# Performance work log

Measured on AMD Instinct MI355X. Metric: run time of the kernel, lower is better.

The kernel has to match this reference:

```python
import jax, jax.numpy as jnp
import numpy as np

N_NODES = 100000


def setup_inputs() -> dict:
    key = jax.random.key(0)
    k1, k2, k3, k4 = jax.random.split(key, 4)
    E = 1600000
    D_IN, D_OUT = 256, 256
    feat = jax.random.normal(k1, (N_NODES, D_IN), dtype=jnp.float32)
    src = jax.random.randint(k2, (E,), 0, N_NODES, dtype=jnp.int32)
    dst = jax.random.randint(k3, (E,), 0, N_NODES, dtype=jnp.int32)
    # xavier_uniform-like init for weight
    limit = np.sqrt(6.0 / (D_IN + D_OUT)).astype(np.float32)
    weight = jax.random.uniform(k4, (D_IN, D_OUT), dtype=jnp.float32,
                                minval=-limit, maxval=limit)
    bias = jnp.zeros((D_OUT,), dtype=jnp.float32)
    return {"feat": feat, "src": src, "dst": dst, "weight": weight, "bias": bias}


def reference(feat, src, dst, weight, bias):
    ones = jnp.ones(src.shape[0], dtype=feat.dtype)
    # out_degrees: number of outgoing edges per node (src counts)
    out_deg = jax.ops.segment_sum(ones, src, num_segments=N_NODES)
    # in_degrees: number of incoming edges per node (dst counts)
    in_deg = jax.ops.segment_sum(ones, dst, num_segments=N_NODES)
    # norm == 'both': pre-scale by out_deg^-0.5
    pre = jnp.power(jnp.clip(out_deg, 1.0), -0.5)[:, None]  # [N,1]
    h = feat * pre
    # message passing: copy_src + sum over incoming edges (SpMM)
    agg = jax.ops.segment_sum(h[src], dst, num_segments=N_NODES)  # [N, D_in]
    # dense projection
    rst = agg @ weight  # [N, D_out]
    # post-scale by in_deg^-0.5
    post = jnp.power(jnp.clip(in_deg, 1.0), -0.5)[:, None]
    rst = rst * post + bias
    return rst
```

## Files before the change

kernel.cpp:

```cpp
#include <hip/hip_runtime.h>
#include <hip/hip_bf16.h>
#include <stdint.h>


using short8  = __attribute__((ext_vector_type(8))) short;
using floatx4 = __attribute__((ext_vector_type(4))) float;
using ushort8 = __attribute__((ext_vector_type(8))) unsigned short;

static __device__ __forceinline__ unsigned short f32_to_bf16(float f) {
    unsigned int u = __float_as_uint(f);
    u += 0x7FFFu + ((u >> 16) & 1u);
    return (unsigned short)(u >> 16);
}
static __device__ __forceinline__ float bf2f(unsigned short u) {
    return __uint_as_float((unsigned int)u << 16);
}

__global__ void k_deg(const int* __restrict__ src, const int* __restrict__ dst,
                      int E, int* __restrict__ outc, int* __restrict__ inc) {
    int i = blockIdx.x * blockDim.x + threadIdx.x;
    if (i < E) {
        atomicAdd(&outc[src[i]], 1);
        atomicAdd(&inc[dst[i]], 1);
    }
}

__global__ void k_off(const int* __restrict__ inc, int N, int* __restrict__ total,
                      int* __restrict__ cursor) {
    __shared__ int ss[256];
    __shared__ int sbase;
    int t = threadIdx.x;
    int i = blockIdx.x * 256 + t;
    int d = (i < N) ? inc[i] : 0;
    int v = d;
    ss[t] = v;
    __syncthreads();
    for (int off = 1; off < 256; off <<= 1) {
        int u = (t >= off) ? ss[t - off] : 0;
        __syncthreads();
        v += u;
        ss[t] = v;
        __syncthreads();
    }
    if (t == 255) sbase = atomicAdd(total, v);
    __syncthreads();
    if (i < N) cursor[i] = sbase + (v - d);
}

__global__ void k_fill(const int* __restrict__ src, const int* __restrict__ dst,
                       int E, int* __restrict__ cursor, int* __restrict__ eidx) {
    int i = blockIdx.x * blockDim.x + threadIdx.x;
    if (i < E) {
        int p = atomicAdd(&cursor[dst[i]], 1);
        eidx[p] = src[i];
    }
}

__global__ void k_wt(const float* __restrict__ W, unsigned short* __restrict__ WT) {
    int i = blockIdx.x * blockDim.x + threadIdx.x;
    int n = i >> 8, k = i & 255;
    WT[n * 256 + k] = f32_to_bf16(W[(size_t)k * 256 + n]);
}

__global__ void __launch_bounds__(512, 4)
k_gemm(const float* __restrict__ feat, const int* __restrict__ outc,
       const unsigned short* __restrict__ WT, int N,
       unsigned short* __restrict__ z) {
    __shared__ unsigned short ldsB[256 * 128];

    int tid  = threadIdx.x;
    int wave = tid >> 6;
    int lane = tid & 63;
    int rl   = lane & 15;
    int g    = lane >> 4;
    int wm0  = blockIdx.x * 128 + wave * 16;
    int rowc = min(wm0 + rl, N - 1);
    float p  = rsqrtf((float)max(outc[rowc], 1));
    const float4* arow = (const float4*)(feat + (size_t)rowc * 256);
    int smask = (rl & 7) << 4;

    floatx4 acc[16];
#pragma unroll
    for (int n = 0; n < 16; ++n) acc[n] = (floatx4){0.f, 0.f, 0.f, 0.f};

#pragma unroll
    for (int h = 0; h < 2; ++h) {
        if (h) __syncthreads();
#pragma unroll
        for (int i = 0; i < 8; ++i) {
            int c    = i * 512 + tid;
            int r2   = c >> 4;
            int colb = (c & 15) << 4;
            ushort8 v = *(const ushort8*)(WT + r2 * 256 + h * 128 + (colb >> 1));
            int dst = r2 * 128 + ((colb ^ ((r2 & 7) << 4)) >> 1);
            *(ushort8*)(&ldsB[dst]) = v;
        }
        __syncthreads();

#pragma unroll
        for (int k2 = 0; k2 < 4; ++k2) {
            float4 v0 = arow[h * 32 + k2 * 8 + g * 2];
            float4 v1 = arow[h * 32 + k2 * 8 + g * 2 + 1];
            short8 a;
            a[0] = (short)f32_to_bf16(v0.x * p);
            a[1] = (short)f32_to_bf16(v0.y * p);
            a[2] = (short)f32_to_bf16(v0.z * p);
            a[3] = (short)f32_to_bf16(v0.w * p);
            a[4] = (short)f32_to_bf16(v1.x * p);
            a[5] = (short)f32_to_bf16(v1.y * p);
            a[6] = (short)f32_to_bf16(v1.z * p);
            a[7] = (short)f32_to_bf16(v1.w * p);
            int cb = (k2 * 64 + g * 16) ^ smask;
#pragma unroll
            for (int n = 0; n < 16; ++n) {
                short8 b = *(const short8*)(&ldsB[(n * 16 + rl) * 128 + (cb >> 1)]);
                acc[n] = __builtin_amdgcn_mfma_f32_16x16x32_bf16(a, b, acc[n], 0, 0, 0);
            }
        }
    }

#pragma unroll
    for (int i = 0; i < 4; ++i) {
        int rw = wm0 + g * 4 + i;
        if (rw < N) {
            ushort8 u0, u1;
#pragma unroll
            for (int j = 0; j < 8; ++j) {
                u0[j] = f32_to_bf16(acc[j][i]);
                u1[j] = f32_to_bf16(acc[8 + j][i]);
            }
            *(ushort8*)(z + (size_t)rw * 256 + rl * 16)     = u0;
            *(ushort8*)(z + (size_t)rw * 256 + rl * 16 + 8) = u1;
        }
    }
}

__global__ void k_agg(const unsigned short* __restrict__ z,
                      const int* __restrict__ cursor, const int* __restrict__ inc,
                      const int* __restrict__ eidx, const float* __restrict__ bias,
                      int N, float* __restrict__ out) {
    int node = blockIdx.x * 4 + (threadIdx.x >> 6);
    if (node >= N) return;
    int lane = threadIdx.x & 63;
    int half = lane >> 5;
    int l = lane & 31;
    int deg = inc[node];
    const int* ep = eidx + (cursor[node] - deg);

    float acc[8];
#pragma unroll
    for (int j = 0; j < 8; ++j) acc[j] = 0.f;

    int e = 0;
    for (; e + 1 < deg; e += 2) {
        int s = ep[e + half];
        ushort8 v = *(const ushort8*)(z + (size_t)s * 256 + l * 8);
#pragma unroll
        for (int j = 0; j < 8; ++j) acc[j] += bf2f(v[j]);
    }
    if (e < deg && half == 0) {
        int s = ep[e];
        ushort8 v = *(const ushort8*)(z + (size_t)s * 256 + l * 8);
#pragma unroll
        for (int j = 0; j < 8; ++j) acc[j] += bf2f(v[j]);
    }
#pragma unroll
    for (int j = 0; j < 8; ++j) acc[j] += __shfl_xor(acc[j], 32);

    float post = rsqrtf((float)max(deg, 1));
#pragma unroll
    for (int jj = 0; jj < 4; ++jj) {
        int pcol = l * 8 + half * 4 + jj;
        int c = ((pcol & 15) << 4) | (pcol >> 4);
        out[(size_t)node * 256 + c] = acc[half * 4 + jj] * post + bias[c];
    }
}

extern "C" void kernel_launch(void* const* d_in, const int* in_sizes, int n_in,
                              void* d_out, int out_size, void* d_ws, size_t ws_size,
                              hipStream_t stream) {
    const float* feat = (const float*)d_in[0];
    const int*   src  = (const int*)d_in[1];
    const int*   dst  = (const int*)d_in[2];
    const float* W    = (const float*)d_in[3];
    const float* bias = (const float*)d_in[4];
    float* out = (float*)d_out;

    const int D = 256;
    int N = in_sizes[0] / D;
    int E = in_sizes[1];

    char* ws = (char*)d_ws;
    size_t off = 0;
    auto alloc = [&](size_t bytes) -> void* {
        void* p = ws + off;
        off += (bytes + 255) & ~(size_t)255;
        return p;
    };
    int*            cnt    = (int*)alloc(((size_t)2 * N + 64) * sizeof(int));
    int*            outc   = cnt;
    int*            inc    = cnt + N;
    int*            total  = cnt + 2 * N;
    int*            cursor = (int*)alloc((size_t)N * sizeof(int));
    int*            eidx   = (int*)alloc((size_t)E * sizeof(int));
    unsigned short* z      = (unsigned short*)alloc((size_t)N * D * sizeof(unsigned short));
    unsigned short* WT     = (unsigned short*)alloc((size_t)D * D * sizeof(unsigned short));
    (void)ws_size;

    hipMemsetAsync(cnt, 0, ((size_t)2 * N + 64) * sizeof(int), stream);

    k_deg <<<(E + 255) / 256, 256, 0, stream>>>(src, dst, E, outc, inc);
    k_off <<<(N + 255) / 256, 256, 0, stream>>>(inc, N, total, cursor);
    k_fill<<<(E + 255) / 256, 256, 0, stream>>>(src, dst, E, cursor, eidx);
    k_wt  <<<(D * D) / 256, 256, 0, stream>>>(W, WT);
    k_gemm<<<(N + 127) / 128, 512, 0, stream>>>(feat, outc, WT, N, z);
    k_agg <<<(N + 3) / 4, 256, 0, stream>>>(z, cursor, inc, eidx, bias, N, out);
}
```

Before: 566.8 us.

## Vectorize edge kernels, split aggregation by column half, change z layout and nontemporal IO

```diff
diff --git a/kernel.cpp b/kernel.cpp
--- a/kernel.cpp
+++ b/kernel.cpp
@@ -5,6 +5,7 @@
 
 using short8  = __attribute__((ext_vector_type(8))) short;
 using floatx4 = __attribute__((ext_vector_type(4))) float;
+using floatx2 = __attribute__((ext_vector_type(2))) float;
 using ushort8 = __attribute__((ext_vector_type(8))) unsigned short;
 
 static __device__ __forceinline__ unsigned short f32_to_bf16(float f) {
@@ -19,9 +20,23 @@
 __global__ void k_deg(const int* __restrict__ src, const int* __restrict__ dst,
                       int E, int* __restrict__ outc, int* __restrict__ inc) {
     int i = blockIdx.x * blockDim.x + threadIdx.x;
-    if (i < E) {
-        atomicAdd(&outc[src[i]], 1);
-        atomicAdd(&inc[dst[i]], 1);
+    int b = i * 4;
+    if (b + 3 < E) {
+        int4 s = *(const int4*)(src + b);
+        int4 d = *(const int4*)(dst + b);
+        atomicAdd(&outc[s.x], 1);
+        atomicAdd(&outc[s.y], 1);
+        atomicAdd(&outc[s.z], 1);
+        atomicAdd(&outc[s.w], 1);
+        atomicAdd(&inc[d.x], 1);
+        atomicAdd(&inc[d.y], 1);
+        atomicAdd(&inc[d.z], 1);
+        atomicAdd(&inc[d.w], 1);
+    } else {
+        for (int j = b; j < E; ++j) {
+            atomicAdd(&outc[src[j]], 1);
+            atomicAdd(&inc[dst[j]], 1);
+        }
     }
 }
 
@@ -50,9 +65,23 @@
 __global__ void k_fill(const int* __restrict__ src, const int* __restrict__ dst,
                        int E, int* __restrict__ cursor, int* __restrict__ eidx) {
     int i = blockIdx.x * blockDim.x + threadIdx.x;
-    if (i < E) {
-        int p = atomicAdd(&cursor[dst[i]], 1);
-        eidx[p] = src[i];
+    int b = i * 4;
+    if (b + 3 < E) {
+        int4 s = *(const int4*)(src + b);
+        int4 d = *(const int4*)(dst + b);
+        int p0 = atomicAdd(&cursor[d.x], 1);
+        int p1 = atomicAdd(&cursor[d.y], 1);
+        int p2 = atomicAdd(&cursor[d.z], 1);
+        int p3 = atomicAdd(&cursor[d.w], 1);
+        eidx[p0] = s.x;
+        eidx[p1] = s.y;
+        eidx[p2] = s.z;
+        eidx[p3] = s.w;
+    } else {
+        for (int j = b; j < E; ++j) {
+            int p = atomicAdd(&cursor[dst[j]], 1);
+            eidx[p] = src[j];
+        }
     }
 }
 
@@ -76,7 +105,7 @@
     int wm0  = blockIdx.x * 128 + wave * 16;
     int rowc = min(wm0 + rl, N - 1);
     float p  = rsqrtf((float)max(outc[rowc], 1));
-    const float4* arow = (const float4*)(feat + (size_t)rowc * 256);
+    const floatx4* arow = (const floatx4*)(feat + (size_t)rowc * 256);
     int smask = (rl & 7) << 4;
 
     floatx4 acc[16];
@@ -99,17 +128,17 @@
 
 #pragma unroll
         for (int k2 = 0; k2 < 4; ++k2) {
-            float4 v0 = arow[h * 32 + k2 * 8 + g * 2];
-            float4 v1 = arow[h * 32 + k2 * 8 + g * 2 + 1];
+            floatx4 v0 = __builtin_nontemporal_load(arow + h * 32 + k2 * 8 + g * 2);
+            floatx4 v1 = __builtin_nontemporal_load(arow + h * 32 + k2 * 8 + g * 2 + 1);
             short8 a;
-            a[0] = (short)f32_to_bf16(v0.x * p);
-            a[1] = (short)f32_to_bf16(v0.y * p);
-            a[2] = (short)f32_to_bf16(v0.z * p);
-            a[3] = (short)f32_to_bf16(v0.w * p);
-            a[4] = (short)f32_to_bf16(v1.x * p);
-            a[5] = (short)f32_to_bf16(v1.y * p);
-            a[6] = (short)f32_to_bf16(v1.z * p);
-            a[7] = (short)f32_to_bf16(v1.w * p);
+            a[0] = (short)f32_to_bf16(v0[0] * p);
+            a[1] = (short)f32_to_bf16(v0[1] * p);
+            a[2] = (short)f32_to_bf16(v0[2] * p);
+            a[3] = (short)f32_to_bf16(v0[3] * p);
+            a[4] = (short)f32_to_bf16(v1[0] * p);
+            a[5] = (short)f32_to_bf16(v1[1] * p);
+            a[6] = (short)f32_to_bf16(v1[2] * p);
+            a[7] = (short)f32_to_bf16(v1[3] * p);
             int cb = (k2 * 64 + g * 16) ^ smask;
 #pragma unroll
             for (int n = 0; n < 16; ++n) {
@@ -120,17 +149,12 @@
     }
 
 #pragma unroll
-    for (int i = 0; i < 4; ++i) {
-        int rw = wm0 + g * 4 + i;
-        if (rw < N) {
-            ushort8 u0, u1;
-#pragma unroll
-            for (int j = 0; j < 8; ++j) {
-                u0[j] = f32_to_bf16(acc[j][i]);
-                u1[j] = f32_to_bf16(acc[8 + j][i]);
-            }
-            *(ushort8*)(z + (size_t)rw * 256 + rl * 16)     = u0;
-            *(ushort8*)(z + (size_t)rw * 256 + rl * 16 + 8) = u1;
+    for (int n = 0; n < 16; ++n) {
+        int c = n * 16 + rl;
+#pragma unroll
+        for (int i = 0; i < 4; ++i) {
+            int rw = wm0 + g * 4 + i;
+            if (rw < N) z[(size_t)rw * 256 + c] = f32_to_bf16(acc[n][i]);
         }
     }
 }
@@ -141,39 +165,51 @@
                       int N, float* __restrict__ out) {
     int node = blockIdx.x * 4 + (threadIdx.x >> 6);
     if (node >= N) return;
+    int h    = blockIdx.y;
     int lane = threadIdx.x & 63;
-    int half = lane >> 5;
-    int l = lane & 31;
-    int deg = inc[node];
+    int q    = lane >> 4;
+    int sl   = lane & 15;
+    int deg  = inc[node];
     const int* ep = eidx + (cursor[node] - deg);
-
-    float acc[8];
-#pragma unroll
-    for (int j = 0; j < 8; ++j) acc[j] = 0.f;
+    const unsigned short* zh = z + h * 128 + sl * 8;
+
+    float accA[8], accB[8];
+#pragma unroll
+    for (int j = 0; j < 8; ++j) { accA[j] = 0.f; accB[j] = 0.f; }
 
     int e = 0;
-    for (; e + 1 < deg; e += 2) {
-        int s = ep[e + half];
-        ushort8 v = *(const ushort8*)(z + (size_t)s * 256 + l * 8);
-#pragma unroll
-        for (int j = 0; j < 8; ++j) acc[j] += bf2f(v[j]);
-    }
-    if (e < deg && half == 0) {
-        int s = ep[e];
-        ushort8 v = *(const ushort8*)(z + (size_t)s * 256 + l * 8);
-#pragma unroll
-        for (int j = 0; j < 8; ++j) acc[j] += bf2f(v[j]);
-    }
-#pragma unroll
-    for (int j = 0; j < 8; ++j) acc[j] += __shfl_xor(acc[j], 32);
+    for (; e + 8 <= deg; e += 8) {
+        int s0 = ep[e + q];
+        int s1 = ep[e + 4 + q];
+        ushort8 v0 = *(const ushort8*)(zh + (size_t)s0 * 256);
+        ushort8 v1 = *(const ushort8*)(zh + (size_t)s1 * 256);
+#pragma unroll
+        for (int j = 0; j < 8; ++j) {
+            accA[j] += bf2f(v0[j]);
+            accB[j] += bf2f(v1[j]);
+        }
+    }
+    for (; e < deg; e += 4) {
+        if (e + q < deg) {
+            int s = ep[e + q];
+            ushort8 v = *(const ushort8*)(zh + (size_t)s * 256);
+#pragma unroll
+            for (int j = 0; j < 8; ++j) accA[j] += bf2f(v[j]);
+        }
+    }
+#pragma unroll
+    for (int j = 0; j < 8; ++j) accA[j] += accB[j];
+#pragma unroll
+    for (int j = 0; j < 8; ++j) accA[j] += __shfl_xor(accA[j], 16);
+#pragma unroll
+    for (int j = 0; j < 8; ++j) accA[j] += __shfl_xor(accA[j], 32);
 
     float post = rsqrtf((float)max(deg, 1));
-#pragma unroll
-    for (int jj = 0; jj < 4; ++jj) {
-        int pcol = l * 8 + half * 4 + jj;
-        int c = ((pcol & 15) << 4) | (pcol >> 4);
-        out[(size_t)node * 256 + c] = acc[half * 4 + jj] * post + bias[c];
-    }
+    int c = h * 128 + sl * 8 + q * 2;
+    floatx2 o;
+    o[0] = accA[q * 2 + 0] * post + bias[c];
+    o[1] = accA[q * 2 + 1] * post + bias[c + 1];
+    __builtin_nontemporal_store(o, (floatx2*)(out + (size_t)node * 256 + c));
 }
 
 extern "C" void kernel_launch(void* const* d_in, const int* in_sizes, int n_in,
@@ -209,10 +245,11 @@
 
     hipMemsetAsync(cnt, 0, ((size_t)2 * N + 64) * sizeof(int), stream);
 
-    k_deg <<<(E + 255) / 256, 256, 0, stream>>>(src, dst, E, outc, inc);
+    int tE4 = (E + 3) / 4;
+    k_deg <<<(tE4 + 255) / 256, 256, 0, stream>>>(src, dst, E, outc, inc);
     k_off <<<(N + 255) / 256, 256, 0, stream>>>(inc, N, total, cursor);
-    k_fill<<<(E + 255) / 256, 256, 0, stream>>>(src, dst, E, cursor, eidx);
+    k_fill<<<(tE4 + 255) / 256, 256, 0, stream>>>(src, dst, E, cursor, eidx);
     k_wt  <<<(D * D) / 256, 256, 0, stream>>>(W, WT);
     k_gemm<<<(N + 127) / 128, 512, 0, stream>>>(feat, outc, WT, N, z);
-    k_agg <<<(N + 3) / 4, 256, 0, stream>>>(z, cursor, inc, eidx, bias, N, out);
-}
+    k_agg <<<dim3((N + 3) / 4, 2), 256, 0, stream>>>(z, cursor, inc, eidx, bias, N, out);
+}
```

Result: no change. 568.8 us (+0.4%).
